# Kernel optimization log

Measured on AMD Instinct MI355X. Metric: run time of the kernel, lower is better.

## Reference

```python
import jax, jax.numpy as jnp
import numpy as np

FP8_MAX = 448.0  # float8_e4m3 max finite value


def setup_inputs() -> dict:
    key = jax.random.key(0)
    k1, k2, k3, k4, k5 = jax.random.split(key, 5)
    B, S, IN, OUT = 8, 2048, 2048, 2048
    x = jax.random.normal(k1, (B, S, IN), dtype=jnp.float32)
    weight = jax.random.normal(k2, (OUT, IN), dtype=jnp.float32) * 0.02
    bias = jax.random.normal(k3, (OUT,), dtype=jnp.float32)
    # per-tensor scales, kept positive and away from zero
    scale_in = jax.random.uniform(k4, (1,), dtype=jnp.float32) * 0.09 + 0.01
    scale_w = jax.random.uniform(k5, (1,), dtype=jnp.float32) * 0.09 + 0.01
    return {"x": x, "weight": weight, "bias": bias,
            "scale_in": scale_in, "scale_w": scale_w}


def _fp8_quantize(x, scale):
    # divide by scale, saturate to fp8 range, cast to fp8 e4m3
    q = jnp.clip(x / scale, -FP8_MAX, FP8_MAX)
    return q.astype(jnp.float8_e4m3fn)


def reference(x, weight, bias, scale_in, scale_w):
    # quantize input and weight to fp8 (per-tensor scales)
    xq = _fp8_quantize(x, scale_in)            # [B,S,IN] fp8
    wq = _fp8_quantize(weight, scale_w)        # [OUT,IN] fp8
    # scaled matmul: accumulate in fp32, dequant with scale_a*scale_b, emit fp16
    acc = jnp.einsum('bsk,nk->bsn', xq.astype(jnp.float32), wq.astype(jnp.float32))
    out = (acc * (scale_in[0] * scale_w[0])).astype(jnp.float16)
    out = out + bias.astype(jnp.float16)       # trailing bias add at fp16
    return out
```

## Files before the change

### kernel.cpp

```cpp
#include <hip/hip_runtime.h>
#include <hip/hip_fp16.h>
#include <stdint.h>

#define MDIM 16384
#define NDIM 2048
#define KDIM 2048

typedef __attribute__((ext_vector_type(4))) float f32x4;
typedef __attribute__((ext_vector_type(4))) int   i32x4;
typedef __attribute__((ext_vector_type(8))) int   i32x8;

#if defined(__has_builtin)
#if __has_builtin(__builtin_amdgcn_cvt_pk_fp8_f32)
#define HAVE_CVT_PK_FP8 1
#endif
#endif

__device__ __forceinline__ unsigned f32_to_e4m3(float x) {
    float q = fminf(448.f, fmaxf(-448.f, x));
    unsigned ub = __float_as_uint(q);
    unsigned sgn = (ub >> 24) & 0x80u;
    float aq = fabsf(q);
    int E = (int)((__float_as_uint(aq) >> 23) & 0xff) - 127;
    if (E < -6) E = -6;
    float rq = __uint_as_float((unsigned)(130 - E) << 23);
    int m = (int)rintf(aq * rq);
    if (m == 16) { m = 8; E += 1; }
    unsigned bits;
    if (m < 8) bits = sgn | (unsigned)m;
    else       bits = sgn | ((unsigned)(E + 7) << 3) | (unsigned)(m - 8);
    return bits;
}

__device__ __forceinline__ uint32_t pack4_e4m3(float a, float b, float c, float d) {
#ifdef HAVE_CVT_PK_FP8
    int r = __builtin_amdgcn_cvt_pk_fp8_f32(a, b, 0, false);
    r = __builtin_amdgcn_cvt_pk_fp8_f32(c, d, r, true);
    return (uint32_t)r;
#else
    return f32_to_e4m3(a) | (f32_to_e4m3(b) << 8) |
           (f32_to_e4m3(c) << 16) | (f32_to_e4m3(d) << 24);
#endif
}

__global__ void quant_both_kernel(const float* __restrict__ x,
                                  uint8_t* __restrict__ xq,
                                  const float* __restrict__ w,
                                  uint8_t* __restrict__ wq,
                                  const float* __restrict__ s_in,
                                  const float* __restrict__ s_w) {
    if (blockIdx.x < 2048) {
        float sc = s_in[0];
        unsigned n16 = (unsigned)((size_t)MDIM * KDIM / 16);
        unsigned i = blockIdx.x * 256 + threadIdx.x;
        for (; i < n16; i += 2048 * 256) {
            const float4* xp = (const float4*)(x + (size_t)i * 16);
            uint32_t wd[4];
#pragma unroll
            for (int j = 0; j < 4; ++j) {
                float4 v = xp[j];
                wd[j] = pack4_e4m3(v.x / sc, v.y / sc, v.z / sc, v.w / sc);
            }
            ((uint4*)xq)[i] = make_uint4(wd[0], wd[1], wd[2], wd[3]);
        }
    } else {
        float sc = s_w[0];
        unsigned n16 = (unsigned)((size_t)NDIM * KDIM / 16);
        unsigned i = (blockIdx.x - 2048) * 256 + threadIdx.x;
        for (; i < n16; i += 256 * 256) {
            const float4* xp = (const float4*)(w + (size_t)i * 16);
            uint32_t wd[4];
#pragma unroll
            for (int j = 0; j < 4; ++j) {
                float4 v = xp[j];
                wd[j] = pack4_e4m3(v.x / sc, v.y / sc, v.z / sc, v.w / sc);
            }
            unsigned r = i >> 7, kc = i & 127;
            unsigned idx = ((r >> 4) * 16 + (kc >> 3)) * 128 +
                           ((kc & 7) >> 1) * 32 + (r & 15) * 2 + (kc & 1);
            ((uint4*)wq)[idx] = make_uint4(wd[0], wd[1], wd[2], wd[3]);
        }
    }
}

#define BM 256
#define BN 256
#define BKB 128
#define NKT (KDIM / BKB)

__device__ __forceinline__ void gload_lds16(const uint8_t* g, uint8_t* l) {
    __builtin_amdgcn_global_load_lds(
        (const __attribute__((address_space(1))) void*)g,
        (__attribute__((address_space(3))) void*)l, 16, 0, 0);
}

__device__ __forceinline__ void barrier_raw() {
    asm volatile("" ::: "memory");
    __builtin_amdgcn_s_barrier();
    asm volatile("" ::: "memory");
}

__global__ __launch_bounds__(512, 2) void gemm_fp8_kernel(
    const uint8_t* __restrict__ Aq, const uint8_t* __restrict__ Bp,
    const float* __restrict__ bias, const float* __restrict__ s_in,
    const float* __restrict__ s_w, float* __restrict__ out) {

    extern __shared__ uint8_t lds[];

    int nwg = gridDim.x;
    int cpx = nwg >> 3;
    int bid = blockIdx.x;
    int swz = (bid & 7) * cpx + (bid >> 3);
    int tm = swz >> 3;
    int tn = swz & 7;
    int row0 = tm * BM;
    int col0 = tn * BN;

    int tid  = threadIdx.x;
    int lane = tid & 63;
    int wid  = tid >> 6;
    int wr = wid >> 2, wc = wid & 3;
    int r15 = lane & 15;
    int g   = lane >> 4;

    int perm0 = ((2 * g + r15) & 7) << 4;
    int perm1 = ((2 * g + 1 + r15) & 7) << 4;

    int ssrc[4], sdst[4];
#pragma unroll
    for (int i = 0; i < 4; ++i) {
        int p = i * 512 + tid;
        int lrow = p >> 3;
        int c = ((p & 7) - (lrow & 7)) & 7;
        ssrc[i] = lrow * KDIM + c * 16;
        sdst[i] = p * 16;
    }
    const uint8_t* Asrc = Aq + (size_t)row0 * KDIM;

#define STAGE_A(KT, BUF)                                                      \
    {                                                                         \
        _Pragma("unroll")                                                     \
        for (int j_ = 0; j_ < 4; ++j_)                                        \
            gload_lds16(Asrc + ssrc[j_] + (size_t)(KT) * BKB, (BUF) + sdst[j_]); \
    }

    const uint8_t* bfbase[4];
#pragma unroll
    for (int n = 0; n < 4; ++n) {
        int n16g = tn * 16 + wc * 4 + n;
        bfbase[n] = Bp + (size_t)n16g * 32768 + lane * 32;
    }

#define LOAD_BF1(DST, N, KT)                                                  \
    {                                                                         \
        const uint8_t* p_ = bfbase[N] + (size_t)(KT) * 2048;                  \
        i32x4 lo = *(const i32x4*)p_;                                         \
        i32x4 hi = *(const i32x4*)(p_ + 16);                                  \
        _Pragma("unroll")                                                     \
        for (int q_ = 0; q_ < 4; ++q_) { DST[q_] = lo[q_]; DST[4 + q_] = hi[q_]; } \
    }

    int aRow0 = wr * 128 + r15;

#define LOAD_AF1(DST, bo, M)                                                  \
    {                                                                         \
        const uint8_t* rp = lds + (bo) + (aRow0 + (M) * 16) * 128;            \
        i32x4 lo = *(const i32x4*)(rp + perm0);                               \
        i32x4 hi = *(const i32x4*)(rp + perm1);                               \
        _Pragma("unroll")                                                     \
        for (int q_ = 0; q_ < 4; ++q_) { DST[q_] = lo[q_]; DST[4 + q_] = hi[q_]; } \
    }

#define MFMA4(AF, M)                                                          \
    __builtin_amdgcn_s_setprio(1);                                            \
    acc[M][0] = __builtin_amdgcn_mfma_scale_f32_16x16x128_f8f6f4(             \
        AF, bf0, acc[M][0], 0, 0, 0, 127, 0, 127);                            \
    acc[M][1] = __builtin_amdgcn_mfma_scale_f32_16x16x128_f8f6f4(             \
        AF, bf1, acc[M][1], 0, 0, 0, 127, 0, 127);                            \
    acc[M][2] = __builtin_amdgcn_mfma_scale_f32_16x16x128_f8f6f4(             \
        AF, bf2, acc[M][2], 0, 0, 0, 127, 0, 127);                            \
    acc[M][3] = __builtin_amdgcn_mfma_scale_f32_16x16x128_f8f6f4(             \
        AF, bf3, acc[M][3], 0, 0, 0, 127, 0, 127);                            \
    __builtin_amdgcn_s_setprio(0);

    f32x4 acc[8][4];
#pragma unroll
    for (int m = 0; m < 8; ++m)
#pragma unroll
        for (int n = 0; n < 4; ++n)
            acc[m][n] = (f32x4){0.f, 0.f, 0.f, 0.f};

    i32x8 bf0, bf1, bf2, bf3;

    uint8_t* buf0 = &lds[0];
    uint8_t* buf1 = &lds[32768];

    STAGE_A(0, buf0);
    asm volatile("s_waitcnt vmcnt(0)" ::: "memory");
    barrier_raw();

#define TILE_BODY(T)                                                          \
    {                                                                         \
        const unsigned bo = ((unsigned)(T) & 1) << 15;                        \
        uint8_t* nxt_ = (((T) & 1) ? buf0 : buf1);                            \
        LOAD_BF1(bf0, 0, T); LOAD_BF1(bf1, 1, T);                             \
        LOAD_BF1(bf2, 2, T); LOAD_BF1(bf3, 3, T);                             \
        asm volatile("" ::: "memory");    \
        if ((T) + 1 < NKT) STAGE_A((T) + 1, nxt_);                            \
        i32x8 afE, afO;                                                       \
        LOAD_AF1(afE, bo, 0);                                                 \
        LOAD_AF1(afO, bo, 1); MFMA4(afE, 0);                                  \
        LOAD_AF1(afE, bo, 2); MFMA4(afO, 1);                                  \
        LOAD_AF1(afO, bo, 3); MFMA4(afE, 2);                                  \
        LOAD_AF1(afE, bo, 4); MFMA4(afO, 3);                                  \
        LOAD_AF1(afO, bo, 5); MFMA4(afE, 4);                                  \
        LOAD_AF1(afE, bo, 6); MFMA4(afO, 5);                                  \
        LOAD_AF1(afO, bo, 7); MFMA4(afE, 6);                                  \
                              MFMA4(afO, 7);                                  \
        asm volatile("s_waitcnt vmcnt(0)" ::: "memory");   \
        barrier_raw();                                                        \
    }

    for (int t = 0; t < NKT; ++t)
        TILE_BODY(t);

    float s = s_in[0] * s_w[0];
    float* slab = (float*)lds;
    __half hb[4];
#pragma unroll
    for (int n = 0; n < 4; ++n)
        hb[n] = __float2half(bias[col0 + wc * 64 + n * 16 + r15]);

#pragma unroll
    for (int q = 0; q < 4; ++q) {
        if (wr == (q >> 1)) {
            const int mh = q & 1;
#pragma unroll
            for (int n = 0; n < 4; ++n) {
                int colb = wc * 64 + n * 16 + r15;
#pragma unroll
                for (int m = 0; m < 4; ++m) {
                    int sr = m * 16 + g * 4;
#pragma unroll
                    for (int r = 0; r < 4; ++r) {
                        __half h = __float2half(acc[mh * 4 + m][n][r] * s);
                        slab[(sr + r) * 256 + colb] = __half2float(__hadd(h, hb[n]));
                    }
                }
            }
        }
        barrier_raw();
#pragma unroll
        for (int it = 0; it < 8; ++it) {
            int srow = wid * 8 + it;
            f32x4 vv = *(const f32x4*)&slab[srow * 256 + lane * 4];
            int grow = row0 + q * 64 + srow;
            *(f32x4*)&out[(size_t)grow * NDIM + col0 + lane * 4] = vv;
        }
        barrier_raw();
    }
#undef STAGE_A
#undef LOAD_BF1
#undef LOAD_AF1
#undef MFMA4
#undef TILE_BODY
}

extern "C" void kernel_launch(void* const* d_in, const int* in_sizes, int n_in,
                              void* d_out, int out_size, void* d_ws, size_t ws_size,
                              hipStream_t stream) {
    const float* x      = (const float*)d_in[0];
    const float* weight = (const float*)d_in[1];
    const float* bias   = (const float*)d_in[2];
    const float* s_in   = (const float*)d_in[3];
    const float* s_w    = (const float*)d_in[4];
    float* out          = (float*)d_out;

    uint8_t* xq = (uint8_t*)d_ws;
    uint8_t* wq = (uint8_t*)d_ws + (size_t)MDIM * KDIM;

    quant_both_kernel<<<2304, 256, 0, stream>>>(x, xq, weight, wq, s_in, s_w);

    dim3 grid((MDIM / BM) * (NDIM / BN));
    gemm_fp8_kernel<<<grid, 512, 65536, stream>>>(xq, wq, bias, s_in, s_w, out);
}
```

Measured before the change: 121.3 us.

## Shrink GEMM tile to 128x256 with 4 waves and prefetch B fragments

The block tile shrinks from 256x256 with 8 waves to 128x256 with 4 waves. Each wave now covers 64x128 (4x8 MFMA tiles) instead of 128x64, so each A fragment read from LDS is reused across 8 B fragments. B fragments for the next K tile are now loaded from global memory after the current MFMAs run, with a partial vmcnt wait, so those loads overlap with the barrier and the next iteration. LDS use halves and the grid doubles, which may raise occupancy. The cost is more registers for the B fragments and more total A and B traffic from the smaller M tile.

```diff
diff --git a/kernel.cpp b/kernel.cpp
--- a/kernel.cpp
+++ b/kernel.cpp
@@ -83,7 +83,7 @@
     }
 }
 
-#define BM 256
+#define BM 128
 #define BN 256
 #define BKB 128
 #define NKT (KDIM / BKB)
@@ -100,7 +100,7 @@
     asm volatile("" ::: "memory");
 }
 
-__global__ __launch_bounds__(512, 2) void gemm_fp8_kernel(
+__global__ __launch_bounds__(256, 2) void gemm_fp8_kernel(
     const uint8_t* __restrict__ Aq, const uint8_t* __restrict__ Bp,
     const float* __restrict__ bias, const float* __restrict__ s_in,
     const float* __restrict__ s_w, float* __restrict__ out) {
@@ -119,7 +119,7 @@
     int tid  = threadIdx.x;
     int lane = tid & 63;
     int wid  = tid >> 6;
-    int wr = wid >> 2, wc = wid & 3;
+    int wr = wid >> 1, wc = wid & 1;
     int r15 = lane & 15;
     int g   = lane >> 4;
 
@@ -129,7 +129,7 @@
     int ssrc[4], sdst[4];
 #pragma unroll
     for (int i = 0; i < 4; ++i) {
-        int p = i * 512 + tid;
+        int p = i * 256 + tid;
         int lrow = p >> 3;
         int c = ((p & 7) - (lrow & 7)) & 7;
         ssrc[i] = lrow * KDIM + c * 16;
@@ -144,23 +144,24 @@
             gload_lds16(Asrc + ssrc[j_] + (size_t)(KT) * BKB, (BUF) + sdst[j_]); \
     }
 
-    const uint8_t* bfbase[4];
-#pragma unroll
-    for (int n = 0; n < 4; ++n) {
-        int n16g = tn * 16 + wc * 4 + n;
-        bfbase[n] = Bp + (size_t)n16g * 32768 + lane * 32;
-    }
+    const uint8_t* Bbase = Bp + (size_t)(tn * 16 + wc * 8) * 32768 + lane * 32;
 
 #define LOAD_BF1(DST, N, KT)                                                  \
     {                                                                         \
-        const uint8_t* p_ = bfbase[N] + (size_t)(KT) * 2048;                  \
+        const uint8_t* p_ = Bbase + (size_t)(N) * 32768 + (size_t)(KT) * 2048; \
         i32x4 lo = *(const i32x4*)p_;                                         \
         i32x4 hi = *(const i32x4*)(p_ + 16);                                  \
         _Pragma("unroll")                                                     \
         for (int q_ = 0; q_ < 4; ++q_) { DST[q_] = lo[q_]; DST[4 + q_] = hi[q_]; } \
     }
 
-    int aRow0 = wr * 128 + r15;
+#define LOAD_BF_ALL(KT)                                                       \
+    LOAD_BF1(bf0, 0, KT); LOAD_BF1(bf1, 1, KT);                               \
+    LOAD_BF1(bf2, 2, KT); LOAD_BF1(bf3, 3, KT);                               \
+    LOAD_BF1(bf4, 4, KT); LOAD_BF1(bf5, 5, KT);                               \
+    LOAD_BF1(bf6, 6, KT); LOAD_BF1(bf7, 7, KT);
+
+    int aRow0 = wr * 64 + r15;
 
 #define LOAD_AF1(DST, bo, M)                                                  \
     {                                                                         \
@@ -171,7 +172,7 @@
         for (int q_ = 0; q_ < 4; ++q_) { DST[q_] = lo[q_]; DST[4 + q_] = hi[q_]; } \
     }
 
-#define MFMA4(AF, M)                                                          \
+#define MFMA8(AF, M)                                                          \
     __builtin_amdgcn_s_setprio(1);                                            \
     acc[M][0] = __builtin_amdgcn_mfma_scale_f32_16x16x128_f8f6f4(             \
         AF, bf0, acc[M][0], 0, 0, 0, 127, 0, 127);                            \
@@ -181,43 +182,52 @@
         AF, bf2, acc[M][2], 0, 0, 0, 127, 0, 127);                            \
     acc[M][3] = __builtin_amdgcn_mfma_scale_f32_16x16x128_f8f6f4(             \
         AF, bf3, acc[M][3], 0, 0, 0, 127, 0, 127);                            \
+    acc[M][4] = __builtin_amdgcn_mfma_scale_f32_16x16x128_f8f6f4(             \
+        AF, bf4, acc[M][4], 0, 0, 0, 127, 0, 127);                            \
+    acc[M][5] = __builtin_amdgcn_mfma_scale_f32_16x16x128_f8f6f4(             \
+        AF, bf5, acc[M][5], 0, 0, 0, 127, 0, 127);                            \
+    acc[M][6] = __builtin_amdgcn_mfma_scale_f32_16x16x128_f8f6f4(             \
+        AF, bf6, acc[M][6], 0, 0, 0, 127, 0, 127);                            \
+    acc[M][7] = __builtin_amdgcn_mfma_scale_f32_16x16x128_f8f6f4(             \
+        AF, bf7, acc[M][7], 0, 0, 0, 127, 0, 127);                            \
     __builtin_amdgcn_s_setprio(0);
 
-    f32x4 acc[8][4];
-#pragma unroll
-    for (int m = 0; m < 8; ++m)
-#pragma unroll
-        for (int n = 0; n < 4; ++n)
+    f32x4 acc[4][8];
+#pragma unroll
+    for (int m = 0; m < 4; ++m)
+#pragma unroll
+        for (int n = 0; n < 8; ++n)
             acc[m][n] = (f32x4){0.f, 0.f, 0.f, 0.f};
 
-    i32x8 bf0, bf1, bf2, bf3;
+    i32x8 bf0, bf1, bf2, bf3, bf4, bf5, bf6, bf7;
 
     uint8_t* buf0 = &lds[0];
-    uint8_t* buf1 = &lds[32768];
+    uint8_t* buf1 = &lds[16384];
 
     STAGE_A(0, buf0);
-    asm volatile("s_waitcnt vmcnt(0)" ::: "memory");
+    asm volatile("" ::: "memory");
+    LOAD_BF_ALL(0);
+    asm volatile("s_waitcnt vmcnt(16)" ::: "memory");
     barrier_raw();
 
 #define TILE_BODY(T)                                                          \
     {                                                                         \
-        const unsigned bo = ((unsigned)(T) & 1) << 15;                        \
+        const unsigned bo = ((unsigned)(T) & 1) << 14;                        \
         uint8_t* nxt_ = (((T) & 1) ? buf0 : buf1);                            \
-        LOAD_BF1(bf0, 0, T); LOAD_BF1(bf1, 1, T);                             \
-        LOAD_BF1(bf2, 2, T); LOAD_BF1(bf3, 3, T);                             \
-        asm volatile("" ::: "memory");    \
-        if ((T) + 1 < NKT) STAGE_A((T) + 1, nxt_);                            \
+        if ((T) + 1 < NKT) STAGE_A((T) + 1, nxt_);     \
+        asm volatile("" ::: "memory");                                        \
         i32x8 afE, afO;                                                       \
-        LOAD_AF1(afE, bo, 0);                                                 \
-        LOAD_AF1(afO, bo, 1); MFMA4(afE, 0);                                  \
-        LOAD_AF1(afE, bo, 2); MFMA4(afO, 1);                                  \
-        LOAD_AF1(afO, bo, 3); MFMA4(afE, 2);                                  \
-        LOAD_AF1(afE, bo, 4); MFMA4(afO, 3);                                  \
-        LOAD_AF1(afO, bo, 5); MFMA4(afE, 4);                                  \
-        LOAD_AF1(afE, bo, 6); MFMA4(afO, 5);                                  \
-        LOAD_AF1(afO, bo, 7); MFMA4(afE, 6);                                  \
-                              MFMA4(afO, 7);                                  \
-        asm volatile("s_waitcnt vmcnt(0)" ::: "memory");   \
+        LOAD_AF1(afE, bo, 0);          \
+        LOAD_AF1(afO, bo, 1); MFMA8(afE, 0);                                  \
+        LOAD_AF1(afE, bo, 2); MFMA8(afO, 1);                                  \
+        LOAD_AF1(afO, bo, 3); MFMA8(afE, 2);                                  \
+                              MFMA8(afO, 3);                                  \
+        if ((T) + 1 < NKT) {                                                  \
+            LOAD_BF_ALL((T) + 1);                \
+            asm volatile("s_waitcnt vmcnt(16)" ::: "memory");  \
+        } else {                                                              \
+            asm volatile("s_waitcnt vmcnt(0)" ::: "memory");                  \
+        }                                                                     \
         barrier_raw();                                                        \
     }
 
@@ -226,24 +236,24 @@
 
     float s = s_in[0] * s_w[0];
     float* slab = (float*)lds;
-    __half hb[4];
-#pragma unroll
-    for (int n = 0; n < 4; ++n)
-        hb[n] = __float2half(bias[col0 + wc * 64 + n * 16 + r15]);
+    __half hb[8];
+#pragma unroll
+    for (int n = 0; n < 8; ++n)
+        hb[n] = __float2half(bias[col0 + wc * 128 + n * 16 + r15]);
 
 #pragma unroll
     for (int q = 0; q < 4; ++q) {
         if (wr == (q >> 1)) {
-            const int mh = q & 1;
-#pragma unroll
-            for (int n = 0; n < 4; ++n) {
-                int colb = wc * 64 + n * 16 + r15;
-#pragma unroll
-                for (int m = 0; m < 4; ++m) {
-                    int sr = m * 16 + g * 4;
+            const int mbase = 2 * (q & 1);
+#pragma unroll
+            for (int n = 0; n < 8; ++n) {
+                int colb = wc * 128 + n * 16 + r15;
+#pragma unroll
+                for (int mm = 0; mm < 2; ++mm) {
+                    int sr = mm * 16 + g * 4;
 #pragma unroll
                     for (int r = 0; r < 4; ++r) {
-                        __half h = __float2half(acc[mh * 4 + m][n][r] * s);
+                        __half h = __float2half(acc[mbase + mm][n][r] * s);
                         slab[(sr + r) * 256 + colb] = __half2float(__hadd(h, hb[n]));
                     }
                 }
@@ -254,15 +264,16 @@
         for (int it = 0; it < 8; ++it) {
             int srow = wid * 8 + it;
             f32x4 vv = *(const f32x4*)&slab[srow * 256 + lane * 4];
-            int grow = row0 + q * 64 + srow;
+            int grow = row0 + q * 32 + srow;
             *(f32x4*)&out[(size_t)grow * NDIM + col0 + lane * 4] = vv;
         }
         barrier_raw();
     }
 #undef STAGE_A
 #undef LOAD_BF1
+#undef LOAD_BF_ALL
 #undef LOAD_AF1
-#undef MFMA4
+#undef MFMA8
 #undef TILE_BODY
 }
 
@@ -282,5 +293,5 @@
     quant_both_kernel<<<2304, 256, 0, stream>>>(x, xq, weight, wq, s_in, s_w);
 
     dim3 grid((MDIM / BM) * (NDIM / BN));
-    gemm_fp8_kernel<<<grid, 512, 65536, stream>>>(xq, wq, bias, s_in, s_w, out);
-}
+    gemm_fp8_kernel<<<grid, 256, 32768, stream>>>(xq, wq, bias, s_in, s_w, out);
+}
```

New measurement: 111.8 us. 1.08x faster.
